# Optimization experiments

Measured on AMD Instinct MI355X. Metric: run time of the kernel, lower is better.

## Reference

```python
import jax, jax.numpy as jnp
from jax import lax
import numpy as np

_MAX_SQRT_GRADIENT = 1000.0

@jax.custom_vjp
def sqrt_bound_derivative(x):
    return jnp.sqrt(x)

def _sbd_fwd(x):
    return jnp.sqrt(x), x

def _sbd_bwd(x, g):
    clipped = jnp.clip(4.0 * x, 1.0 / _MAX_SQRT_GRADIENT**2)
    return (g / jnp.sqrt(clipped),)

sqrt_bound_derivative.defvjp(_sbd_fwd, _sbd_bwd)

HIDDEN = 2560
LRU = 2560
HEADS = 10
CONV_W = 4
BATCH = 2
SEQ = 4096


def setup_inputs() -> dict:
    key = jax.random.key(0)
    ks = jax.random.split(key, 12)
    s = 0.02  # init scale for weights
    inp = {
        'input_states': jax.random.normal(ks[0], (BATCH, SEQ, HIDDEN), jnp.float32),
        'position_ids': jnp.broadcast_to(jnp.arange(SEQ, dtype=jnp.int64), (BATCH, SEQ)),
        'prev_h': jnp.zeros((BATCH, LRU), jnp.float32),
        'w_y': jax.random.normal(ks[1], (LRU, HIDDEN), jnp.float32) * s,
        'b_y': jax.random.normal(ks[2], (LRU,), jnp.float32) * s,
        'w_x': jax.random.normal(ks[3], (LRU, HIDDEN), jnp.float32) * s,
        'b_x': jax.random.normal(ks[4], (LRU,), jnp.float32) * s,
        'w_out': jax.random.normal(ks[5], (HIDDEN, LRU), jnp.float32) * s,
        'b_out': jax.random.normal(ks[6], (HIDDEN,), jnp.float32) * s,
        'conv_w': jax.random.normal(ks[7], (LRU, CONV_W), jnp.float32) * 0.3,
        'conv_b': jax.random.normal(ks[8], (LRU,), jnp.float32) * s,
        'a_param': jax.random.normal(ks[9], (LRU,), jnp.float32),
        'ig_w': jax.random.normal(ks[10], (LRU // HEADS, LRU), jnp.float32) * s,
        'ig_b': jnp.zeros((LRU // HEADS,), jnp.float32),
        'ag_w': jax.random.normal(ks[11], (LRU // HEADS, LRU), jnp.float32) * s,
        'ag_b': jnp.zeros((LRU // HEADS,), jnp.float32),
    }
    return inp


def _block_gate(x_bshi, gate_w, gate_b, heads, bw):
    # gate_w is the nn.Linear weight [bw, heads*bw] reshaped to block-diagonal form
    w = gate_w.reshape(heads, bw, bw).transpose(0, 2, 1)  # h i j
    y = jnp.einsum('bshi,hij->bshj', x_bshi, w) + gate_b
    B, S = y.shape[0], y.shape[1]
    return jax.nn.sigmoid(y.reshape(B, S, heads * bw))


def _rglru(activations, position_ids, prev_h, a_param, ig_w, ig_b, ag_w, ag_b):
    B, S, D = activations.shape
    bw = ig_w.shape[0]
    heads = ig_w.shape[1] // bw
    reset = (position_ids[:, :, None] == 0)  # [B,S,1] bool
    x = activations.reshape(B, S, heads, bw)
    gate_x = _block_gate(x, ig_w, ig_b, heads, bw)  # [B,S,D]
    gate_a = _block_gate(x, ag_w, ag_b, heads, bw)  # [B,S,D]
    log_a = -8.0 * gate_a * jax.nn.softplus(a_param)
    a = jnp.exp(log_a)
    a_square = jnp.exp(2.0 * log_a)
    gated_x = activations * gate_x
    multiplier = sqrt_bound_derivative(1.0 - a_square)
    multiplier = jnp.where(reset, 1.0, multiplier)
    normalized_x = gated_x * multiplier.astype(activations.dtype)
    a = a * (~reset)  # zero the decay at document boundaries

    def step(h, inp):
        a_t, x_t = inp  # [B,D] each
        h = a_t.astype(jnp.float32) * h + x_t.astype(jnp.float32)
        return h, h.astype(activations.dtype)

    xs = (a.transpose(1, 0, 2), normalized_x.transpose(1, 0, 2))  # time-major
    last_h, y = lax.scan(step, prev_h, xs)
    return y.transpose(1, 0, 2), last_h


def reference(input_states, position_ids, prev_h, w_y, b_y, w_x, b_x,
              w_out, b_out, conv_w, conv_b, a_param, ig_w, ig_b, ag_w, ag_b):
    B, S, _ = input_states.shape
    # y branch: gelu(tanh approx)
    y_branch = jax.nn.gelu(input_states @ w_y.T + b_y, approximate=True)
    # x branch: linear + depthwise causal conv (kernel width CONV_W)
    x_branch = input_states @ w_x.T + b_x  # [B,S,LRU]
    Wd = conv_w.shape[1]
    xp = jnp.pad(x_branch, ((0, 0), (Wd - 1, 0), (0, 0)))
    conv_out = conv_b + sum(xp[:, k:k + S, :] * conv_w[:, k] for k in range(Wd))
    # RG-LRU
    h, last_h = _rglru(conv_out, position_ids, prev_h, a_param, ig_w, ig_b, ag_w, ag_b)
    h = h * y_branch
    out = h @ w_out.T + b_out
    return out
```

## Files before the change

kernel.cpp:

```cpp
#include <hip/hip_runtime.h>
#include <hip/hip_bf16.h>
#include <math.h>

typedef __hip_bfloat16 bf16;
typedef __attribute__((ext_vector_type(4))) float f32x4;
typedef __attribute__((ext_vector_type(8))) __bf16 bf16x8;

static constexpr int HID    = 2560;
static constexpr int LRUD   = 2560;
static constexpr int HEADSN = 10;
static constexpr int BWID   = 256;
static constexpr int SEQL   = 4096;
static constexpr int BATCHN = 2;
static constexpr int NTOK   = BATCHN * SEQL;
static constexpr int NCHUNK = 128;
static constexpr int CHLEN  = 32;

#define GAS __attribute__((address_space(1)))
#define LAS __attribute__((address_space(3)))
#define MEMFENCE asm volatile("" ::: "memory")
#define PHASE_SYNC                                        \
  __builtin_amdgcn_s_barrier(); MEMFENCE;                 \
  asm volatile("s_waitcnt lgkmcnt(0)" ::: "memory");
#define PHASE_END                                         \
  __builtin_amdgcn_s_barrier(); MEMFENCE;
#define VMGATE6 asm volatile("s_waitcnt vmcnt(6)" ::: "memory")
#define VMGATE0 asm volatile("s_waitcnt vmcnt(0)" ::: "memory")
#define LGKM8   asm volatile("s_waitcnt lgkmcnt(8)" ::: "memory")

__device__ __forceinline__ void async_copy16(void* lds, const void* g) {
  __builtin_amdgcn_global_load_lds((const GAS unsigned int*)g,
                                   (LAS unsigned int*)lds, 16, 0, 0);
}

template<int EPI>
__global__ __launch_bounds__(512, 2)
void gemm256_kernel(const bf16* __restrict__ A, int lda,
                    const bf16* __restrict__ B0p, const bf16* __restrict__ B1p,
                    int ldb,
                    const float* __restrict__ bias0, const float* __restrict__ bias1,
                    void* __restrict__ out0, void* __restrict__ out1,
                    int ldc, int K)
{
  __shared__ __align__(16) bf16 As[2][256 * 64];
  __shared__ __align__(16) bf16 Bs[2][256 * 64];

  const int tid  = threadIdx.x;
  const int wave = tid >> 6;
  const int lane = tid & 63;
  const int wm   = wave >> 2;
  const int wn   = wave & 3;

  const int nxy  = gridDim.x * gridDim.y;
  const int orig = blockIdx.y * gridDim.x + blockIdx.x;
  const int swz  = (orig & 7) * (nxy >> 3) + (orig >> 3);
  const int m0   = (swz / gridDim.x) * 256;
  const int n0   = (swz % gridDim.x) * 256;

  const int zsel = (EPI == 1) ? (int)blockIdx.z : 0;
  const bf16*  Bw   = zsel ? B1p : B0p;
  const float* bias = zsel ? bias1 : bias0;

  const int NT = K / 64;
  f32x4  acc[8][4] = {};
  bf16x8 a[4][2], bl[2][2], bh[2][2];

  const int srow = tid >> 3;
  const int spb  = (tid & 7) * 16;
  const int scb  = spb ^ ((srow & 7) << 4);

  const int lrow = lane & 15;
  const int swzc = (lane & 7) << 4;
  const int col0 = ((lane >> 4) * 16) ^ swzc;
  const int col1 = (64 + (lane >> 4) * 16) ^ swzc;
  const char* aBase = (const char*)&As[0][0] + (wm * 128 + lrow) * 128;
  const char* bBase = (const char*)&Bs[0][0] + (wn * 64 + lrow) * 128;
  constexpr int BUFB = 256 * 64 * 2;

  auto stageA = [&](int t, int c) {
    const int r = c * 64 + srow;
    async_copy16(&As[t & 1][c * 4096 + wave * 512],
                 A + (size_t)(m0 + r) * lda + t * 64 + (scb >> 1));
  };
  auto stageB = [&](int t, int c) {
    const int r = c * 64 + srow;
    async_copy16(&Bs[t & 1][c * 4096 + wave * 512],
                 Bw + (size_t)(n0 + r) * ldb + t * 64 + (scb >> 1));
  };
  auto stA_lo = [&](int t) { stageA(t, 0); stageA(t, 2); };
  auto stA_hi = [&](int t) { stageA(t, 1); stageA(t, 3); };
  auto stB01  = [&](int t) { stageB(t, 0); stageB(t, 1); };
  auto stB23  = [&](int t) { stageB(t, 2); stageB(t, 3); };

  auto readAhalf = [&](int buf, int half) {
    const char* p = aBase + buf * BUFB + half * 4 * 2048;
#pragma unroll
    for (int j = 0; j < 4; ++j) {
      a[j][0] = *(const bf16x8*)(p + j * 2048 + col0);
      a[j][1] = *(const bf16x8*)(p + j * 2048 + col1);
    }
  };
  auto readBlo = [&](int buf) {
    const char* p = bBase + buf * BUFB;
#pragma unroll
    for (int f = 0; f < 2; ++f) {
      bl[f][0] = *(const bf16x8*)(p + f * 2048 + col0);
      bl[f][1] = *(const bf16x8*)(p + f * 2048 + col1);
    }
  };
  auto readBhi = [&](int buf) {
    const char* p = bBase + buf * BUFB + 2 * 2048;
#pragma unroll
    for (int f = 0; f < 2; ++f) {
      bh[f][0] = *(const bf16x8*)(p + f * 2048 + col0);
      bh[f][1] = *(const bf16x8*)(p + f * 2048 + col1);
    }
  };
  auto mfmaQ = [&](int fmB, int fnB, bf16x8 (&bx)[2][2]) {
#pragma unroll
    for (int ks = 0; ks < 2; ++ks)
#pragma unroll
      for (int fn = 0; fn < 2; ++fn)
#pragma unroll
        for (int fm = 0; fm < 4; ++fm)
          acc[fmB + fm][fnB + fn] = __builtin_amdgcn_mfma_f32_16x16x32_bf16(
              a[fm][ks], bx[fn][ks], acc[fmB + fm][fnB + fn], 0, 0, 0);
  };

  stA_lo(0); stB01(0); stB23(0); stA_hi(0);
  stA_lo(1); stB01(1); stB23(1);
  VMGATE6;
  PHASE_END;

  const int NI = NT / 2;
  for (int i = 0; i < NI; ++i) {
    const int  t0 = 2 * i, t1 = 2 * i + 1;
    const bool s2 = (t0 + 2) < NT;

    readAhalf(0, 0); readBlo(0);
    stA_hi(t1);
    LGKM8;
    PHASE_SYNC;
    __builtin_amdgcn_s_setprio(1); mfmaQ(0, 0, bl); __builtin_amdgcn_s_setprio(0);
    PHASE_END;
    readBhi(0);
    if (s2) stA_lo(t0 + 2);
    PHASE_SYNC;
    __builtin_amdgcn_s_setprio(1); mfmaQ(0, 2, bh); __builtin_amdgcn_s_setprio(0);
    PHASE_END;
    readAhalf(0, 1);
    if (s2) stB01(t0 + 2);
    PHASE_SYNC;
    __builtin_amdgcn_s_setprio(1); mfmaQ(4, 2, bh); __builtin_amdgcn_s_setprio(0);
    PHASE_END;
    if (s2) stB23(t0 + 2);
    PHASE_SYNC;
    __builtin_amdgcn_s_setprio(1); mfmaQ(4, 0, bl); __builtin_amdgcn_s_setprio(0);
    if (s2) { VMGATE6; } else { VMGATE0; }
    PHASE_END;
    readAhalf(1, 0); readBlo(1);
    if (s2) stA_hi(t0 + 2);
    LGKM8;
    PHASE_SYNC;
    __builtin_amdgcn_s_setprio(1); mfmaQ(0, 0, bl); __builtin_amdgcn_s_setprio(0);
    PHASE_END;
    readBhi(1);
    if (s2) stA_lo(t1 + 2);
    PHASE_SYNC;
    __builtin_amdgcn_s_setprio(1); mfmaQ(0, 2, bh); __builtin_amdgcn_s_setprio(0);
    PHASE_END;
    readAhalf(1, 1);
    if (s2) stB01(t1 + 2);
    PHASE_SYNC;
    __builtin_amdgcn_s_setprio(1); mfmaQ(4, 2, bh); __builtin_amdgcn_s_setprio(0);
    PHASE_END;
    if (s2) stB23(t1 + 2);
    PHASE_SYNC;
    __builtin_amdgcn_s_setprio(1); mfmaQ(4, 0, bl); __builtin_amdgcn_s_setprio(0);
    if (s2) { VMGATE6; }
    PHASE_END;
  }

  const int mrb = (lane >> 4) * 4;
  const int ncc = lane & 15;
#pragma unroll
  for (int fm = 0; fm < 8; ++fm) {
#pragma unroll
    for (int fn = 0; fn < 4; ++fn) {
      const int n  = n0 + wn * 64 + fn * 16 + ncc;
      const float bv = bias[n];
#pragma unroll
      for (int r = 0; r < 4; ++r) {
        const int m = m0 + wm * 128 + fm * 16 + mrb + r;
        const size_t idx = (size_t)m * ldc + n;
        float v = acc[fm][fn][r] + bv;
        if constexpr (EPI == 0) {
          ((float*)out0)[idx] = v;
        } else {
          if (zsel == 0) {
            const float t = tanhf(0.7978845608028654f * (v + 0.044715f * v * v * v));
            ((bf16*)out0)[idx] = __float2bfloat16(0.5f * v * (1.0f + t));
          } else {
            ((bf16*)out1)[idx] = __float2bfloat16(v);
          }
        }
      }
    }
  }
}

__global__ __launch_bounds__(256)
void gemm128_f32_kernel(const bf16* __restrict__ A, int lda,
                        const bf16* __restrict__ Bw, int ldb,
                        const float* __restrict__ bias,
                        float* __restrict__ C, int ldc, int K)
{
  __shared__ __align__(16) bf16 As[128 * 64];
  __shared__ __align__(16) bf16 Bs[128 * 64];

  const int tid  = threadIdx.x;
  const int wave = tid >> 6;
  const int lane = tid & 63;
  const int wy   = wave >> 1;
  const int wx   = wave & 1;
  const int m0   = blockIdx.y * 128;
  const int n0   = blockIdx.x * 128;

  f32x4 acc[4][4] = {};
  const int srow = tid >> 3;
  const int spb  = (tid & 7) * 16;
  const int scb  = spb ^ ((srow & 7) << 4);

  const int lrow = lane & 15;
  const int swzc = (lane & 7) << 4;
  const int col0 = ((lane >> 4) * 16) ^ swzc;
  const int col1 = (64 + (lane >> 4) * 16) ^ swzc;
  const char* aBase = (const char*)As + (wy * 64 + lrow) * 128;
  const char* bBase = (const char*)Bs + (wx * 64 + lrow) * 128;

  for (int k0 = 0; k0 < K; k0 += 64) {
#pragma unroll
    for (int rd = 0; rd < 4; ++rd) {
      const int r = rd * 32 + srow;
      async_copy16(&As[rd * 2048 + wave * 512],
                   A + (size_t)(m0 + r) * lda + k0 + (scb >> 1));
      async_copy16(&Bs[rd * 2048 + wave * 512],
                   Bw + (size_t)(n0 + r) * ldb + k0 + (scb >> 1));
    }
    __syncthreads();
#pragma unroll
    for (int ks = 0; ks < 2; ++ks) {
      const int colk = ks ? col1 : col0;
      bf16x8 af[4], bfr[4];
#pragma unroll
      for (int f = 0; f < 4; ++f) {
        af[f]  = *(const bf16x8*)(aBase + f * 2048 + colk);
        bfr[f] = *(const bf16x8*)(bBase + f * 2048 + colk);
      }
#pragma unroll
      for (int fm = 0; fm < 4; ++fm)
#pragma unroll
        for (int fn = 0; fn < 4; ++fn)
          acc[fm][fn] = __builtin_amdgcn_mfma_f32_16x16x32_bf16(af[fm], bfr[fn], acc[fm][fn], 0, 0, 0);
    }
    __syncthreads();
  }

  const int mrb = (lane >> 4) * 4;
  const int ncc = lane & 15;
#pragma unroll
  for (int fm = 0; fm < 4; ++fm) {
#pragma unroll
    for (int fn = 0; fn < 4; ++fn) {
      const int n  = n0 + wx * 64 + fn * 16 + ncc;
      const float bv = bias[n];
#pragma unroll
      for (int r = 0; r < 4; ++r) {
        const int m = m0 + wy * 64 + fm * 16 + mrb + r;
        C[(size_t)m * ldc + n] = acc[fm][fn][r] + bv;
      }
    }
  }
}

__global__ __launch_bounds__(256)
void gate_gemm_kernel(const bf16* __restrict__ Conv,
                      const bf16* __restrict__ IGb, const bf16* __restrict__ AGb,
                      const float* __restrict__ ig_b, const float* __restrict__ ag_b,
                      bf16* __restrict__ Gx, bf16* __restrict__ Ga)
{
  __shared__ __align__(16) bf16 As[128 * 64];
  __shared__ __align__(16) bf16 Bs[128 * 64];

  const int tid  = threadIdx.x;
  const int wave = tid >> 6;
  const int lane = tid & 63;
  const int wy   = wave >> 1;
  const int wx   = wave & 1;
  const int m0   = blockIdx.y * 128;
  const int n0   = blockIdx.x * 128;
  const int head = blockIdx.z % HEADSN;
  const int sel  = blockIdx.z / HEADSN;

  const bf16*  A    = Conv + head * BWID;
  const bf16*  Bw   = (sel ? AGb : IGb) + (size_t)head * BWID * BWID;
  const float* bias = sel ? ag_b : ig_b;
  bf16*        Cp   = (sel ? Ga : Gx) + head * BWID;

  f32x4 acc[4][4] = {};
  const int srow = tid >> 3;
  const int spb  = (tid & 7) * 16;
  const int scb  = spb ^ ((srow & 7) << 4);

  const int lrow = lane & 15;
  const int swzc = (lane & 7) << 4;
  const int col0 = ((lane >> 4) * 16) ^ swzc;
  const int col1 = (64 + (lane >> 4) * 16) ^ swzc;
  const char* aBase = (const char*)As + (wy * 64 + lrow) * 128;
  const char* bBase = (const char*)Bs + (wx * 64 + lrow) * 128;

  for (int k0 = 0; k0 < BWID; k0 += 64) {
#pragma unroll
    for (int rd = 0; rd < 4; ++rd) {
      const int r = rd * 32 + srow;
      async_copy16(&As[rd * 2048 + wave * 512],
                   A + (size_t)(m0 + r) * LRUD + k0 + (scb >> 1));
      async_copy16(&Bs[rd * 2048 + wave * 512],
                   Bw + (size_t)(n0 + r) * BWID + k0 + (scb >> 1));
    }
    __syncthreads();
#pragma unroll
    for (int ks = 0; ks < 2; ++ks) {
      const int colk = ks ? col1 : col0;
      bf16x8 af[4], bfr[4];
#pragma unroll
      for (int f = 0; f < 4; ++f) {
        af[f]  = *(const bf16x8*)(aBase + f * 2048 + colk);
        bfr[f] = *(const bf16x8*)(bBase + f * 2048 + colk);
      }
#pragma unroll
      for (int fm = 0; fm < 4; ++fm)
#pragma unroll
        for (int fn = 0; fn < 4; ++fn)
          acc[fm][fn] = __builtin_amdgcn_mfma_f32_16x16x32_bf16(af[fm], bfr[fn], acc[fm][fn], 0, 0, 0);
    }
    __syncthreads();
  }

  const int mrb = (lane >> 4) * 4;
  const int ncc = lane & 15;
#pragma unroll
  for (int fm = 0; fm < 4; ++fm) {
#pragma unroll
    for (int fn = 0; fn < 4; ++fn) {
      const int n  = n0 + wx * 64 + fn * 16 + ncc;
      const float bv = bias[n];
#pragma unroll
      for (int r = 0; r < 4; ++r) {
        const int m = m0 + wy * 64 + fm * 16 + mrb + r;
        float v = acc[fm][fn][r] + bv;
        Cp[(size_t)m * LRUD + n] = __float2bfloat16(1.0f / (1.0f + expf(-v)));
      }
    }
  }
}

static constexpr int CV0 = NTOK * HID / 4;
static constexpr int CVW = LRUD * HID / 4;
static constexpr int CVG = BWID * LRUD / 4;
static constexpr int CVT_TOTAL = CV0 + 3 * CVW + 2 * CVG;

__device__ __forceinline__ void cvt4(const float* src, bf16* dst, int j) {
  const float4 v = *(const float4*)(src + (size_t)j * 4);
  dst[(size_t)j * 4 + 0] = __float2bfloat16(v.x);
  dst[(size_t)j * 4 + 1] = __float2bfloat16(v.y);
  dst[(size_t)j * 4 + 2] = __float2bfloat16(v.z);
  dst[(size_t)j * 4 + 3] = __float2bfloat16(v.w);
}

__global__ __launch_bounds__(256)
void cvt_all_kernel(const float* __restrict__ x_in, const float* __restrict__ w_y,
                    const float* __restrict__ w_x, const float* __restrict__ w_out,
                    const float* __restrict__ ig_w, const float* __restrict__ ag_w,
                    bf16* __restrict__ Xbf, bf16* __restrict__ Wyb,
                    bf16* __restrict__ Wxb, bf16* __restrict__ Wob,
                    bf16* __restrict__ IGb, bf16* __restrict__ AGb)
{
  int g = blockIdx.x * 256 + threadIdx.x;
  if (g < CV0)                       { cvt4(x_in,  Xbf, g); return; }
  g -= CV0;
  if (g < CVW)                       { cvt4(w_y,   Wyb, g); return; }
  g -= CVW;
  if (g < CVW)                       { cvt4(w_x,   Wxb, g); return; }
  g -= CVW;
  if (g < CVW)                       { cvt4(w_out, Wob, g); return; }
  g -= CVW;
  if (g < CVG)                       { cvt4(ig_w,  IGb, g); return; }
  g -= CVG;
  cvt4(ag_w, AGb, g);
}

__global__ __launch_bounds__(256)
void conv_kernel(const bf16* __restrict__ Xb, const float* __restrict__ cw,
                 const float* __restrict__ cbias, bf16* __restrict__ out) {
  const int c  = blockIdx.x * 256 + threadIdx.x;
  const int t0 = blockIdx.y * 8;
  const int bb = blockIdx.z;
  size_t base = ((size_t)bb * SEQL + t0) * LRUD + c;
  const float w0 = cw[c * 4 + 0], w1 = cw[c * 4 + 1];
  const float w2 = cw[c * 4 + 2], w3 = cw[c * 4 + 3];
  const float bc = cbias[c];
  float xm1, xm2, xm3;
  if (blockIdx.y == 0) { xm1 = xm2 = xm3 = 0.f; }
  else {
    xm1 = __bfloat162float(Xb[base - (size_t)LRUD]);
    xm2 = __bfloat162float(Xb[base - (size_t)2 * LRUD]);
    xm3 = __bfloat162float(Xb[base - (size_t)3 * LRUD]);
  }
#pragma unroll
  for (int tl = 0; tl < 8; ++tl) {
    const float x = __bfloat162float(Xb[base]);
    out[base] = __float2bfloat16(bc + x * w3 + xm1 * w2 + xm2 * w1 + xm3 * w0);
    xm3 = xm2; xm2 = xm1; xm1 = x;
    base += LRUD;
  }
}

__device__ __forceinline__ void compute_ax(float conv, float gx, float ga, float sp,
                                           int t, float& a, float& x) {
  const float la  = -8.f * ga * sp;
  a               = expf(la);
  const float asq = expf(2.f * la);
  float mult      = sqrtf(fmaxf(1.f - asq, 0.f));
  if (t == 0) { a = 0.f; mult = 1.f; }
  x = conv * gx * mult;
}

__global__ __launch_bounds__(256)
void scan1_kernel(const bf16* __restrict__ conv, const bf16* __restrict__ gxb,
                  const bf16* __restrict__ gab, const float* __restrict__ a_param,
                  float* __restrict__ cA, float* __restrict__ cX) {
  const int c     = blockIdx.x * 256 + threadIdx.x;
  const int chunk = blockIdx.y;
  const int b     = blockIdx.z;
  const float ap  = a_param[c];
  const float sp  = (ap > 20.f) ? ap : log1pf(expf(ap));
  size_t base = ((size_t)b * SEQL + (size_t)chunk * CHLEN) * LRUD + c;
  float A = 1.f, X = 0.f;
  for (int tl = 0; tl < CHLEN; ++tl) {
    float a, x;
    compute_ax(__bfloat162float(conv[base]), __bfloat162float(gxb[base]),
               __bfloat162float(gab[base]), sp, chunk * CHLEN + tl, a, x);
    X = a * X + x;
    A *= a;
    base += LRUD;
  }
  const size_t ci = ((size_t)b * NCHUNK + chunk) * LRUD + c;
  cA[ci] = A;
  cX[ci] = X;
}

__global__ __launch_bounds__(256)
void scan2_kernel(const float* __restrict__ cA, const float* __restrict__ cX,
                  const float* __restrict__ prev_h, float* __restrict__ pref) {
  const int g = blockIdx.x * 256 + threadIdx.x;
  const int b = g / LRUD;
  const int c = g % LRUD;
  float h = prev_h[g];
#pragma unroll 8
  for (int ch = 0; ch < NCHUNK; ++ch) {
    const size_t ci = ((size_t)b * NCHUNK + ch) * LRUD + c;
    pref[ci] = h;
    h = cA[ci] * h + cX[ci];
  }
}

__global__ __launch_bounds__(256)
void scan3_kernel(const bf16* __restrict__ conv, const bf16* __restrict__ gxb,
                  const bf16* __restrict__ gab, const float* __restrict__ a_param,
                  const float* __restrict__ pref, const bf16* __restrict__ yb,
                  bf16* __restrict__ hm) {
  const int c     = blockIdx.x * 256 + threadIdx.x;
  const int chunk = blockIdx.y;
  const int b     = blockIdx.z;
  const float ap  = a_param[c];
  const float sp  = (ap > 20.f) ? ap : log1pf(expf(ap));
  float h = pref[((size_t)b * NCHUNK + chunk) * LRUD + c];
  size_t base = ((size_t)b * SEQL + (size_t)chunk * CHLEN) * LRUD + c;
  for (int tl = 0; tl < CHLEN; ++tl) {
    float a, x;
    compute_ax(__bfloat162float(conv[base]), __bfloat162float(gxb[base]),
               __bfloat162float(gab[base]), sp, chunk * CHLEN + tl, a, x);
    h = a * h + x;
    hm[base] = __float2bfloat16(h * __bfloat162float(yb[base]));
    base += LRUD;
  }
}

extern "C" void kernel_launch(void* const* d_in, const int* in_sizes, int n_in,
                              void* d_out, int out_size, void* d_ws, size_t ws_size,
                              hipStream_t stream) {
  const float* x_in    = (const float*)d_in[0];
  const float* prev_h  = (const float*)d_in[2];
  const float* w_y     = (const float*)d_in[3];
  const float* b_y     = (const float*)d_in[4];
  const float* w_x     = (const float*)d_in[5];
  const float* b_x     = (const float*)d_in[6];
  const float* w_out   = (const float*)d_in[7];
  const float* b_out   = (const float*)d_in[8];
  const float* conv_w  = (const float*)d_in[9];
  const float* conv_b  = (const float*)d_in[10];
  const float* a_param = (const float*)d_in[11];
  const float* ig_w    = (const float*)d_in[12];
  const float* ig_b    = (const float*)d_in[13];
  const float* ag_w    = (const float*)d_in[14];
  const float* ag_b    = (const float*)d_in[15];

  char* ws = (char*)d_ws;
  size_t off = 0;
  auto alloc = [&](size_t bytes) -> char* {
    char* p = ws + off;
    off += (bytes + 255) & ~(size_t)255;
    return p;
  };
  bf16*  Xbf  = (bf16*)alloc((size_t)NTOK * HID * 2);
  bf16*  Wyb  = (bf16*)alloc((size_t)LRUD * HID * 2);
  bf16*  Wxb  = (bf16*)alloc((size_t)LRUD * HID * 2);
  bf16*  Wob  = (bf16*)alloc((size_t)HID * LRUD * 2);
  bf16*  IGb  = (bf16*)alloc((size_t)BWID * LRUD * 2);
  bf16*  AGb  = (bf16*)alloc((size_t)BWID * LRUD * 2);
  bf16*  Conv = (bf16*)alloc((size_t)NTOK * LRUD * 2);
  float* cA   = (float*)alloc((size_t)BATCHN * NCHUNK * LRUD * 4);
  float* cX   = (float*)alloc((size_t)BATCHN * NCHUNK * LRUD * 4);
  float* pref = (float*)alloc((size_t)BATCHN * NCHUNK * LRUD * 4);

  bf16* Yb = (bf16*)d_out;
  bf16* Xb = (bf16*)d_out + (size_t)NTOK * LRUD;
  bf16* Gx = Xbf;
  bf16* Ga = Xb;
  bf16* Hm = Conv;

  cvt_all_kernel<<<dim3(CVT_TOTAL / 256), 256, 0, stream>>>(
      x_in, w_y, w_x, w_out, ig_w, ag_w, Xbf, Wyb, Wxb, Wob, IGb, AGb);

  gemm256_kernel<1><<<dim3(LRUD / 256, NTOK / 256, 2), 512, 0, stream>>>(
      Xbf, HID, Wyb, Wxb, HID, b_y, b_x, Yb, Xb, LRUD, HID);
  conv_kernel<<<dim3(LRUD / 256, SEQL / 8, BATCHN), 256, 0, stream>>>(
      Xb, conv_w, conv_b, Conv);
  gate_gemm_kernel<<<dim3(BWID / 128, NTOK / 128, 2 * HEADSN), 256, 0, stream>>>(
      Conv, IGb, AGb, ig_b, ag_b, Gx, Ga);
  scan1_kernel<<<dim3(LRUD / 256, NCHUNK, BATCHN), 256, 0, stream>>>(
      Conv, Gx, Ga, a_param, cA, cX);
  scan2_kernel<<<dim3((BATCHN * LRUD) / 256), 256, 0, stream>>>(cA, cX, prev_h, pref);
  scan3_kernel<<<dim3(LRUD / 256, NCHUNK, BATCHN), 256, 0, stream>>>(
      Conv, Gx, Ga, a_param, pref, Yb, Hm);
  gemm128_f32_kernel<<<dim3(HID / 128, NTOK / 128), 256, 0, stream>>>(
      Hm, LRUD, Wob, LRUD, b_out, (float*)d_out, HID, LRUD);

  (void)in_sizes; (void)n_in; (void)out_size; (void)ws_size;
}
```

Before: 568.2 us.

## Shrink pipelined GEMM to 128x128 tiles and reuse it for output projection

The double-buffered, phase-scheduled GEMM is scaled from 256x256 tiles with 512 threads down to 128x128 tiles with 256 threads. It is used for both the fused y/x projection and the output projection, which replaces the simpler single-buffered 128 kernel. The intent is better occupancy and wave count on the fused GEMM, plus overlapped loads in the final GEMM. Smaller tiles cut per-tile reuse and raise global traffic. The lgkmcnt waits are also removed before the barriers.

```diff
diff --git a/kernel.cpp b/kernel.cpp
--- a/kernel.cpp
+++ b/kernel.cpp
@@ -26,7 +26,6 @@
   __builtin_amdgcn_s_barrier(); MEMFENCE;
 #define VMGATE6 asm volatile("s_waitcnt vmcnt(6)" ::: "memory")
 #define VMGATE0 asm volatile("s_waitcnt vmcnt(0)" ::: "memory")
-#define LGKM8   asm volatile("s_waitcnt lgkmcnt(8)" ::: "memory")
 
 __device__ __forceinline__ void async_copy16(void* lds, const void* g) {
   __builtin_amdgcn_global_load_lds((const GAS unsigned int*)g,
@@ -34,36 +33,36 @@
 }
 
 template<int EPI>
-__global__ __launch_bounds__(512, 2)
-void gemm256_kernel(const bf16* __restrict__ A, int lda,
-                    const bf16* __restrict__ B0p, const bf16* __restrict__ B1p,
-                    int ldb,
-                    const float* __restrict__ bias0, const float* __restrict__ bias1,
-                    void* __restrict__ out0, void* __restrict__ out1,
-                    int ldc, int K)
+__global__ __launch_bounds__(256, 2)
+void gemm128q_kernel(const bf16* __restrict__ A, int lda,
+                     const bf16* __restrict__ B0p, const bf16* __restrict__ B1p,
+                     int ldb,
+                     const float* __restrict__ bias0, const float* __restrict__ bias1,
+                     void* __restrict__ out0, void* __restrict__ out1,
+                     int ldc, int K)
 {
-  __shared__ __align__(16) bf16 As[2][256 * 64];
-  __shared__ __align__(16) bf16 Bs[2][256 * 64];
+  __shared__ __align__(16) bf16 As[2][128 * 64];
+  __shared__ __align__(16) bf16 Bs[2][128 * 64];
 
   const int tid  = threadIdx.x;
   const int wave = tid >> 6;
   const int lane = tid & 63;
-  const int wm   = wave >> 2;
-  const int wn   = wave & 3;
+  const int wm   = wave >> 1;
+  const int wn   = wave & 1;
 
   const int nxy  = gridDim.x * gridDim.y;
   const int orig = blockIdx.y * gridDim.x + blockIdx.x;
   const int swz  = (orig & 7) * (nxy >> 3) + (orig >> 3);
-  const int m0   = (swz / gridDim.x) * 256;
-  const int n0   = (swz % gridDim.x) * 256;
+  const int m0   = (swz / gridDim.x) * 128;
+  const int n0   = (swz % gridDim.x) * 128;
 
   const int zsel = (EPI == 1) ? (int)blockIdx.z : 0;
   const bf16*  Bw   = zsel ? B1p : B0p;
   const float* bias = zsel ? bias1 : bias0;
 
   const int NT = K / 64;
-  f32x4  acc[8][4] = {};
-  bf16x8 a[4][2], bl[2][2], bh[2][2];
+  f32x4  acc[4][4] = {};
+  bf16x8 a[2][2], bl[2][2], bh[2][2];
 
   const int srow = tid >> 3;
   const int spb  = (tid & 7) * 16;
@@ -73,29 +72,29 @@
   const int swzc = (lane & 7) << 4;
   const int col0 = ((lane >> 4) * 16) ^ swzc;
   const int col1 = (64 + (lane >> 4) * 16) ^ swzc;
-  const char* aBase = (const char*)&As[0][0] + (wm * 128 + lrow) * 128;
+  const char* aBase = (const char*)&As[0][0] + (wm * 64 + lrow) * 128;
   const char* bBase = (const char*)&Bs[0][0] + (wn * 64 + lrow) * 128;
-  constexpr int BUFB = 256 * 64 * 2;
+  constexpr int BUFB = 128 * 64 * 2;
 
   auto stageA = [&](int t, int c) {
-    const int r = c * 64 + srow;
-    async_copy16(&As[t & 1][c * 4096 + wave * 512],
+    const int r = c * 32 + srow;
+    async_copy16(&As[t & 1][c * 2048 + wave * 512],
                  A + (size_t)(m0 + r) * lda + t * 64 + (scb >> 1));
   };
   auto stageB = [&](int t, int c) {
-    const int r = c * 64 + srow;
-    async_copy16(&Bs[t & 1][c * 4096 + wave * 512],
+    const int r = c * 32 + srow;
+    async_copy16(&Bs[t & 1][c * 2048 + wave * 512],
                  Bw + (size_t)(n0 + r) * ldb + t * 64 + (scb >> 1));
   };
   auto stA_lo = [&](int t) { stageA(t, 0); stageA(t, 2); };
   auto stA_hi = [&](int t) { stageA(t, 1); stageA(t, 3); };
-  auto stB01  = [&](int t) { stageB(t, 0); stageB(t, 1); };
-  auto stB23  = [&](int t) { stageB(t, 2); stageB(t, 3); };
+  auto stB_lo = [&](int t) { stageB(t, 0); stageB(t, 2); };
+  auto stB_hi = [&](int t) { stageB(t, 1); stageB(t, 3); };
 
   auto readAhalf = [&](int buf, int half) {
-    const char* p = aBase + buf * BUFB + half * 4 * 2048;
-#pragma unroll
-    for (int j = 0; j < 4; ++j) {
+    const char* p = aBase + buf * BUFB + half * 2 * 2048;
+#pragma unroll
+    for (int j = 0; j < 2; ++j) {
       a[j][0] = *(const bf16x8*)(p + j * 2048 + col0);
       a[j][1] = *(const bf16x8*)(p + j * 2048 + col1);
     }
@@ -122,13 +121,13 @@
 #pragma unroll
       for (int fn = 0; fn < 2; ++fn)
 #pragma unroll
-        for (int fm = 0; fm < 4; ++fm)
+        for (int fm = 0; fm < 2; ++fm)
           acc[fmB + fm][fnB + fn] = __builtin_amdgcn_mfma_f32_16x16x32_bf16(
               a[fm][ks], bx[fn][ks], acc[fmB + fm][fnB + fn], 0, 0, 0);
   };
 
-  stA_lo(0); stB01(0); stB23(0); stA_hi(0);
-  stA_lo(1); stB01(1); stB23(1);
+  stA_lo(0); stB_lo(0); stB_hi(0); stA_hi(0);
+  stA_lo(1); stB_lo(1); stB_hi(1);
   VMGATE6;
   PHASE_END;
 
@@ -139,7 +138,6 @@
 
     readAhalf(0, 0); readBlo(0);
     stA_hi(t1);
-    LGKM8;
     PHASE_SYNC;
     __builtin_amdgcn_s_setprio(1); mfmaQ(0, 0, bl); __builtin_amdgcn_s_setprio(0);
     PHASE_END;
@@ -149,18 +147,17 @@
     __builtin_amdgcn_s_setprio(1); mfmaQ(0, 2, bh); __builtin_amdgcn_s_setprio(0);
     PHASE_END;
     readAhalf(0, 1);
-    if (s2) stB01(t0 + 2);
-    PHASE_SYNC;
-    __builtin_amdgcn_s_setprio(1); mfmaQ(4, 2, bh); __builtin_amdgcn_s_setprio(0);
-    PHASE_END;
-    if (s2) stB23(t0 + 2);
-    PHASE_SYNC;
-    __builtin_amdgcn_s_setprio(1); mfmaQ(4, 0, bl); __builtin_amdgcn_s_setprio(0);
+    if (s2) stB_lo(t0 + 2);
+    PHASE_SYNC;
+    __builtin_amdgcn_s_setprio(1); mfmaQ(2, 2, bh); __builtin_amdgcn_s_setprio(0);
+    PHASE_END;
+    if (s2) stB_hi(t0 + 2);
+    PHASE_SYNC;
+    __builtin_amdgcn_s_setprio(1); mfmaQ(2, 0, bl); __builtin_amdgcn_s_setprio(0);
     if (s2) { VMGATE6; } else { VMGATE0; }
     PHASE_END;
     readAhalf(1, 0); readBlo(1);
     if (s2) stA_hi(t0 + 2);
-    LGKM8;
     PHASE_SYNC;
     __builtin_amdgcn_s_setprio(1); mfmaQ(0, 0, bl); __builtin_amdgcn_s_setprio(0);
     PHASE_END;
@@ -170,13 +167,13 @@
     __builtin_amdgcn_s_setprio(1); mfmaQ(0, 2, bh); __builtin_amdgcn_s_setprio(0);
     PHASE_END;
     readAhalf(1, 1);
-    if (s2) stB01(t1 + 2);
-    PHASE_SYNC;
-    __builtin_amdgcn_s_setprio(1); mfmaQ(4, 2, bh); __builtin_amdgcn_s_setprio(0);
-    PHASE_END;
-    if (s2) stB23(t1 + 2);
-    PHASE_SYNC;
-    __builtin_amdgcn_s_setprio(1); mfmaQ(4, 0, bl); __builtin_amdgcn_s_setprio(0);
+    if (s2) stB_lo(t1 + 2);
+    PHASE_SYNC;
+    __builtin_amdgcn_s_setprio(1); mfmaQ(2, 2, bh); __builtin_amdgcn_s_setprio(0);
+    PHASE_END;
+    if (s2) stB_hi(t1 + 2);
+    PHASE_SYNC;
+    __builtin_amdgcn_s_setprio(1); mfmaQ(2, 0, bl); __builtin_amdgcn_s_setprio(0);
     if (s2) { VMGATE6; }
     PHASE_END;
   }
@@ -184,14 +181,14 @@
   const int mrb = (lane >> 4) * 4;
   const int ncc = lane & 15;
 #pragma unroll
-  for (int fm = 0; fm < 8; ++fm) {
+  for (int fm = 0; fm < 4; ++fm) {
 #pragma unroll
     for (int fn = 0; fn < 4; ++fn) {
       const int n  = n0 + wn * 64 + fn * 16 + ncc;
       const float bv = bias[n];
 #pragma unroll
       for (int r = 0; r < 4; ++r) {
-        const int m = m0 + wm * 128 + fm * 16 + mrb + r;
+        const int m = m0 + wm * 64 + fm * 16 + mrb + r;
         const size_t idx = (size_t)m * ldc + n;
         float v = acc[fm][fn][r] + bv;
         if constexpr (EPI == 0) {
@@ -204,80 +201,6 @@
             ((bf16*)out1)[idx] = __float2bfloat16(v);
           }
         }
-      }
-    }
-  }
-}
-
-__global__ __launch_bounds__(256)
-void gemm128_f32_kernel(const bf16* __restrict__ A, int lda,
-                        const bf16* __restrict__ Bw, int ldb,
-                        const float* __restrict__ bias,
-                        float* __restrict__ C, int ldc, int K)
-{
-  __shared__ __align__(16) bf16 As[128 * 64];
-  __shared__ __align__(16) bf16 Bs[128 * 64];
-
-  const int tid  = threadIdx.x;
-  const int wave = tid >> 6;
-  const int lane = tid & 63;
-  const int wy   = wave >> 1;
-  const int wx   = wave & 1;
-  const int m0   = blockIdx.y * 128;
-  const int n0   = blockIdx.x * 128;
-
-  f32x4 acc[4][4] = {};
-  const int srow = tid >> 3;
-  const int spb  = (tid & 7) * 16;
-  const int scb  = spb ^ ((srow & 7) << 4);
-
-  const int lrow = lane & 15;
-  const int swzc = (lane & 7) << 4;
-  const int col0 = ((lane >> 4) * 16) ^ swzc;
-  const int col1 = (64 + (lane >> 4) * 16) ^ swzc;
-  const char* aBase = (const char*)As + (wy * 64 + lrow) * 128;
-  const char* bBase = (const char*)Bs + (wx * 64 + lrow) * 128;
-
-  for (int k0 = 0; k0 < K; k0 += 64) {
-#pragma unroll
-    for (int rd = 0; rd < 4; ++rd) {
-      const int r = rd * 32 + srow;
-      async_copy16(&As[rd * 2048 + wave * 512],
-                   A + (size_t)(m0 + r) * lda + k0 + (scb >> 1));
-      async_copy16(&Bs[rd * 2048 + wave * 512],
-                   Bw + (size_t)(n0 + r) * ldb + k0 + (scb >> 1));
-    }
-    __syncthreads();
-#pragma unroll
-    for (int ks = 0; ks < 2; ++ks) {
-      const int colk = ks ? col1 : col0;
-      bf16x8 af[4], bfr[4];
-#pragma unroll
-      for (int f = 0; f < 4; ++f) {
-        af[f]  = *(const bf16x8*)(aBase + f * 2048 + colk);
-        bfr[f] = *(const bf16x8*)(bBase + f * 2048 + colk);
-      }
-#pragma unroll
-      for (int fm = 0; fm < 4; ++fm)
-#pragma unroll
-        for (int fn = 0; fn < 4; ++fn)
-          acc[fm][fn] = __builtin_amdgcn_mfma_f32_16x16x32_bf16(af[fm], bfr[fn], acc[fm][fn], 0, 0, 0);
-    }
-    __syncthreads();
-  }
-
-  const int mrb = (lane >> 4) * 4;
-  const int ncc = lane & 15;
-#pragma unroll
-  for (int fm = 0; fm < 4; ++fm) {
-#pragma unroll
-    for (int fn = 0; fn < 4; ++fn) {
-      const int n  = n0 + wx * 64 + fn * 16 + ncc;
-      const float bv = bias[n];
-#pragma unroll
-      for (int r = 0; r < 4; ++r) {
-        const int m = m0 + wy * 64 + fm * 16 + mrb + r;
-        C[(size_t)m * ldc + n] = acc[fm][fn][r] + bv;
       }
     }
   }
@@ -543,7 +466,7 @@
   cvt_all_kernel<<<dim3(CVT_TOTAL / 256), 256, 0, stream>>>(
       x_in, w_y, w_x, w_out, ig_w, ag_w, Xbf, Wyb, Wxb, Wob, IGb, AGb);
 
-  gemm256_kernel<1><<<dim3(LRUD / 256, NTOK / 256, 2), 512, 0, stream>>>(
+  gemm128q_kernel<1><<<dim3(LRUD / 128, NTOK / 128, 2), 256, 0, stream>>>(
       Xbf, HID, Wyb, Wxb, HID, b_y, b_x, Yb, Xb, LRUD, HID);
   conv_kernel<<<dim3(LRUD / 256, SEQL / 8, BATCHN), 256, 0, stream>>>(
       Xb, conv_w, conv_b, Conv);
@@ -554,8 +477,9 @@
   scan2_kernel<<<dim3((BATCHN * LRUD) / 256), 256, 0, stream>>>(cA, cX, prev_h, pref);
   scan3_kernel<<<dim3(LRUD / 256, NCHUNK, BATCHN), 256, 0, stream>>>(
       Conv, Gx, Ga, a_param, pref, Yb, Hm);
-  gemm128_f32_kernel<<<dim3(HID / 128, NTOK / 128), 256, 0, stream>>>(
-      Hm, LRUD, Wob, LRUD, b_out, (float*)d_out, HID, LRUD);
+  gemm128q_kernel<0><<<dim3(HID / 128, NTOK / 128), 256, 0, stream>>>(
+      Hm, LRUD, Wob, Wob, LRUD, b_out, b_out, (float*)d_out, (float*)d_out,
+      HID, LRUD);
 
   (void)in_sizes; (void)n_in; (void)out_size; (void)ws_size;
 }
```

After: 555.9 us. 1.02x faster.
